# Performance work log

Measured on AMD Instinct MI355X. Metric: run time of the kernel, lower is better.

Reference implementation:

```python
import jax, jax.numpy as jnp
import numpy as np
from jax import lax

SUM_WEIGHT = 1.0
EPS = 1e-5
STRIDE = (2, 2, 2)
PAD = (1, 1, 1)
OUT_PAD = (1, 1, 1)
POOL = (2, 2, 2)


def setup_inputs() -> dict:
    key = jax.random.key(0)
    k1, k2, k3 = jax.random.split(key, 3)
    N, Cin, Cout = 32, 32, 64
    D, H, W = 16, 32, 32
    K = 3
    x = jax.random.normal(k1, (N, Cin, D, H, W), dtype=jnp.float32)
    fan_in = Cin * K * K * K
    w = jax.random.normal(k2, (Cin, Cout, K, K, K), dtype=jnp.float32) / np.sqrt(fan_in)
    b = jax.random.normal(k3, (Cout,), dtype=jnp.float32) * 0.01
    gamma = jnp.ones((Cout,), dtype=jnp.float32)
    beta = jnp.zeros((Cout,), dtype=jnp.float32)
    return {"x": x, "weight": w, "bias": b, "gamma": gamma, "beta": beta}


def _forward(x, weight, bias, gamma, beta):
    K = weight.shape[2]
    # ConvTranspose3d as correlation on stride-dilated input. The CUDA kernel
    # scatters with od = id*s - p + (K-1-kd) using weight[kd], i.e. the
    # spatially-flipped weight vs torch convT -> plain correlation here.
    pad_cfg = [(K - 1 - p, K - 1 - p + op) for p, op in zip(PAD, OUT_PAD)]
    y = lax.conv_general_dilated(
        x, weight,
        window_strides=(1, 1, 1),
        padding=pad_cfg,
        lhs_dilation=STRIDE,
        dimension_numbers=("NCDHW", "IODHW", "NCDHW"),
    )
    y = y + bias[None, :, None, None, None] + SUM_WEIGHT
    # Channel-wise LayerNorm: normalize over C at each (n, d, h, w), biased var.
    mean = jnp.mean(y, axis=1, keepdims=True)
    var = jnp.mean(jnp.square(y - mean), axis=1, keepdims=True)
    y = (y - mean) * lax.rsqrt(var + EPS)
    y = y * gamma[None, :, None, None, None] + beta[None, :, None, None, None]
    # AvgPool3d with kernel == stride == POOL via reshape + mean.
    N, C, Do, Ho, Wo = y.shape
    kd, kh, kw = POOL
    y = y.reshape(N, C, Do // kd, kd, Ho // kh, kh, Wo // kw, kw).mean(axis=(3, 5, 7))
    # GELU, tanh approximation (matches the CUDA kernel constants).
    c0 = jnp.float32(0.7978845608028654)
    c1 = jnp.float32(0.044715)
    return 0.5 * y * (1.0 + jnp.tanh(c0 * (y + c1 * y * y * y)))


def reference(x, weight, bias, gamma, beta):
    return _forward(x, weight, bias, gamma, beta)
```

## Files before the change

### kernel.cpp

```cpp
#include <hip/hip_runtime.h>
#include <math.h>


typedef __attribute__((ext_vector_type(8))) short short8;
typedef __attribute__((ext_vector_type(4))) float f32x4;

__device__ __forceinline__ unsigned short f2bf(float v) {
    unsigned int b = __float_as_uint(v);
    return (unsigned short)((b + 0x7fffu + ((b >> 16) & 1u)) >> 16);
}

__global__ void pack_w(const float* __restrict__ w, unsigned short* __restrict__ wp) {
    int t = blockIdx.x * 256 + threadIdx.x;
    if (t >= 27 * 64 * 32) return;
    int ci = t & 31, co = (t >> 5) & 63, tap = t >> 11;
    wp[(tap * 64 + co) * 32 + ci] = f2bf(w[(ci * 64 + co) * 27 + tap]);
}

__global__ __launch_bounds__(256, 2) void mfma_fused(
    const float* __restrict__ x, const unsigned short* __restrict__ wpack,
    const float* __restrict__ bias, const float* __restrict__ gamma,
    const float* __restrict__ beta, float* __restrict__ out)
{
    constexpr int COFF[9]   = {0, 1, 3, 5, 9, 11, 15, 19, 27};
    constexpr int TAPIDX[27] = {13, 12,14, 10,16, 9,11,15,17,
                                4,22, 3,5,21,23, 1,7,19,25,
                                0,2,6,8,18,20,24,26};
    constexpr int XROW[27]  = {0, 0,1, 0,33, 0,1,33,34,
                               0,99, 0,1,99,100, 0,33,99,132,
                               0,1,33,34,99,100,132,133};

    __shared__ unsigned short xs[6336];
    __shared__ float cbuf[2][64 * 68];

    const int t = threadIdx.x;
    const int lane = t & 63;
    const int wv = t >> 6;
    const int l15 = lane & 15;
    const int quad = lane >> 4;
    const int cobase = wv * 16;

    const int b = blockIdx.x;
    const int bq = b & 3;
    const int dp = (b >> 2) & 15;
    const int n = b >> 6;

    short8 Breg[27];
#pragma unroll
    for (int u = 0; u < 27; ++u)
        Breg[u] = *(const short8*)(wpack + (TAPIDX[u] * 64 + cobase + l15) * 32 + quad * 8);

    int base2[4], swzB[4];
#pragma unroll
    for (int s = 0; s < 4; ++s) {
        int m = s * 16 + l15;
        base2[s] = ((m >> 5) * 33 + (m & 31)) * 64;
    }
#pragma unroll
    for (int k = 0; k < 4; ++k)
        swzB[k] = (quad ^ ((l15 + k) & 3)) << 4;

    const float bco = bias[cobase + l15] + 1.0f;
    const int p = t >> 2, qq = t & 3;
    f32x4 gm[4], bt[4];
#pragma unroll
    for (int jj = 0; jj < 4; ++jj) {
        gm[jj] = *(const f32x4*)(gamma + qq * 16 + jj * 4);
        bt[jj] = *(const f32x4*)(beta + qq * 16 + jj * 4);
    }

    const char* xsb = (const char*)xs;

    for (int it = 0; it < 4; ++it) {
        const int hp0 = (bq * 4 + it) * 2;
        __syncthreads();

        for (int i = t; i < 792; i += 256) {
            int ww = i % 33;
            int g = i / 33;
            int chunk = g & 3;
            int gh = g >> 2;
            int dd = (gh >= 3) ? 1 : 0;
            int hh = gh - dd * 3;
            int row = gh * 33 + ww;
            int id = dp + dd, ih = hp0 + hh;
            short8 v8 = (short8)0;
            if (ww < 32 && ih < 32 && id < 16) {
                const float* xp = x + (((size_t)(n * 32 + chunk * 8) * 16 + id) << 10)
                                    + ih * 32 + ww;
#pragma unroll
                for (int j = 0; j < 8; ++j)
                    v8[j] = (short)f2bf(xp[(size_t)j << 14]);
            }
            *(short8*)((char*)xs + row * 64 + ((chunk ^ (row & 3)) << 4)) = v8;
        }
        __syncthreads();

        float pool[16];
#pragma unroll
        for (int j = 0; j < 16; ++j) pool[j] = 0.f;

#pragma unroll
        for (int c = 0; c < 8; ++c) {
            float* cb = cbuf[c & 1];
            f32x4 acc[4];
#pragma unroll
            for (int s = 0; s < 4; ++s) acc[s] = (f32x4)0.f;

#pragma unroll
            for (int u = COFF[c]; u < COFF[c + 1]; ++u) {
#pragma unroll
                for (int s = 0; s < 4; ++s) {
                    short8 a = *(const short8*)(xsb + base2[s]
                                + swzB[(XROW[u] + (s >> 1)) & 3] + XROW[u] * 64);
                    acc[s] = __builtin_amdgcn_mfma_f32_16x16x32_bf16(a, Breg[u], acc[s], 0, 0, 0);
                }
            }
#pragma unroll
            for (int s = 0; s < 4; ++s)
#pragma unroll
                for (int r = 0; r < 4; ++r)
                    cb[(s * 16 + quad * 4 + r) * 68 + cobase + l15] = acc[s][r] + bco;
            __syncthreads();

            f32x4 vv[4];
#pragma unroll
            for (int jj = 0; jj < 4; ++jj)
                vv[jj] = *(const f32x4*)&cb[p * 68 + qq * 16 + jj * 4];
            float s1 = 0.f, s2 = 0.f;
#pragma unroll
            for (int jj = 0; jj < 4; ++jj)
#pragma unroll
                for (int k = 0; k < 4; ++k) { float v = vv[jj][k]; s1 += v; s2 += v * v; }
            s1 += __shfl_xor(s1, 1); s2 += __shfl_xor(s2, 1);
            s1 += __shfl_xor(s1, 2); s2 += __shfl_xor(s2, 2);
            float mean = s1 * (1.f / 64.f);
            float var = s2 * (1.f / 64.f) - mean * mean;
            float rstd = rsqrtf(var + 1e-5f);
#pragma unroll
            for (int jj = 0; jj < 4; ++jj)
#pragma unroll
                for (int k = 0; k < 4; ++k)
                    pool[jj * 4 + k] += (vv[jj][k] - mean) * rstd;
        }

        float* eb = cbuf[0];
#pragma unroll
        for (int jj = 0; jj < 4; ++jj)
#pragma unroll
            for (int k = 0; k < 4; ++k) {
                float y = pool[jj * 4 + k] * 0.125f * gm[jj][k] + bt[jj][k];
                float u = 0.7978845608028654f * (y + 0.044715f * y * y * y);
                float g = y / (1.f + __expf(-2.f * u));
                eb[(qq * 16 + jj * 4 + k) * 65 + p] = g;
            }
        __syncthreads();
#pragma unroll
        for (int k2 = 0; k2 < 4; ++k2) {
            int idx = k2 * 256 + t;
            int c = idx >> 4;
            int pp = (idx & 15) * 4;
            f32x4 vq = *(const f32x4*)&eb[c * 65 + pp];
            *(f32x4*)&out[(((size_t)(n * 64 + c) * 16 + dp) << 10) + hp0 * 32 + pp] = vq;
        }
    }
}

__global__ __launch_bounds__(256) void fused_fallback(
    const float* __restrict__ x, const float* __restrict__ w,
    const float* __restrict__ bias, const float* __restrict__ gamma,
    const float* __restrict__ beta, float* __restrict__ out)
{
    __shared__ __align__(16) float xs_lds[128 * 20];
    __shared__ float conv_lds[128 * 65];
    float* stats = xs_lds;

    const int t = threadIdx.x;
    const int b = blockIdx.x;
    const int wq = b & 1;
    const int hp = (b >> 1) & 31;
    const int dp = (b >> 6) & 15;
    const int n = b >> 10;

    for (int k = 0; k < 10; ++k) {
        int idx = t + k * 256;
        int col = idx % 20, r = idx / 20;
        int hh = r & 1, ddv = (r >> 1) & 1, ci = r >> 2;
        int iw = wq * 16 + col, ih = hp + hh, id = dp + ddv;
        float v = 0.f;
        if (col < 17 && iw < 32 && ih < 32 && id < 16)
            v = x[(((n * 32 + ci) * 16 + id) * 32 + ih) * 32 + iw];
        xs_lds[idx] = v;
    }
    __syncthreads();

    const int co = t & 63;
    const int sg = t >> 6;
    const float bco = bias[co] + 1.0f;

    for (int dd = 0; dd < 2; ++dd)
        for (int hh = 0; hh < 2; ++hh) {
            float acc[8];
#pragma unroll
            for (int j = 0; j < 8; ++j) acc[j] = 0.f;
            const int ndt = dd ? 2 : 1, nht = hh ? 2 : 1;
            for (int itp = 0; itp < ndt; ++itp) {
                const int kd = dd ? (itp ? 2 : 0) : 1;
                const int idl = dd ? itp : 0;
                for (int jt = 0; jt < nht; ++jt) {
                    const int kh = hh ? (jt ? 2 : 0) : 1;
                    const int ihl = hh ? jt : 0;
                    const int kidx = kd * 3 + kh;
#pragma unroll 4
                    for (int ci = 0; ci < 32; ++ci) {
                        const float* wp0 = w + (ci * 64 + co) * 27 + kidx * 3;
                        float w0 = wp0[0], w1 = wp0[1], w2 = wp0[2];
                        const float* xr = &xs_lds[(ci * 4 + idl * 2 + ihl) * 20 + sg * 4];
                        float4 xa = *(const float4*)xr;
                        float x4 = xr[4];
                        acc[0] += xa.x * w1;
                        acc[1] += xa.x * w0 + xa.y * w2;
                        acc[2] += xa.y * w1;
                        acc[3] += xa.y * w0 + xa.z * w2;
                        acc[4] += xa.z * w1;
                        acc[5] += xa.z * w0 + xa.w * w2;
                        acc[6] += xa.w * w1;
                        acc[7] += xa.w * w0 + x4 * w2;
                    }
                }
            }
            const int posb = (dd * 2 + hh) * 32 + sg * 8;
#pragma unroll
            for (int j = 0; j < 8; ++j)
                conv_lds[(posb + j) * 65 + co] = acc[j] + bco;
        }
    __syncthreads();

    if (t < 128) {
        float s = 0.f, ss = 0.f;
#pragma unroll 8
        for (int c = 0; c < 64; ++c) { float v = conv_lds[t * 65 + c]; s += v; ss += v * v; }
        float mean = s * (1.f / 64.f);
        float var = ss * (1.f / 64.f) - mean * mean;
        stats[t] = mean;
        stats[128 + t] = rsqrtf(var + 1e-5f);
    }
    __syncthreads();

    {
        const int wp = t & 15, cog = t >> 4;
#pragma unroll
        for (int j = 0; j < 4; ++j) {
            const int c = cog * 4 + j;
            float sum = 0.f;
#pragma unroll
            for (int pd2 = 0; pd2 < 4; ++pd2)
#pragma unroll
                for (int ww = 0; ww < 2; ++ww) {
                    const int pos = pd2 * 32 + wp * 2 + ww;
                    sum += (conv_lds[pos * 65 + c] - stats[pos]) * stats[128 + pos];
                }
            float y = sum * 0.125f * gamma[c] + beta[c];
            float u = 0.7978845608028654f * (y + 0.044715f * y * y * y);
            float g = 0.5f * y * (1.f + tanhf(u));
            out[(((n * 64 + c) * 16 + dp) * 32 + hp) * 32 + (wq * 16 + wp)] = g;
        }
    }
}

extern "C" void kernel_launch(void* const* d_in, const int* in_sizes, int n_in,
                              void* d_out, int out_size, void* d_ws, size_t ws_size,
                              hipStream_t stream) {
    const float* x = (const float*)d_in[0];
    const float* w = (const float*)d_in[1];
    const float* bias = (const float*)d_in[2];
    const float* gamma = (const float*)d_in[3];
    const float* beta = (const float*)d_in[4];
    float* out = (float*)d_out;

    const size_t need = (size_t)(27 * 64 * 32) * sizeof(unsigned short);
    if (ws_size >= need) {
        unsigned short* wpack = (unsigned short*)d_ws;
        pack_w<<<(27 * 64 * 32 + 255) / 256, 256, 0, stream>>>(w, wpack);
        mfma_fused<<<2048, 256, 0, stream>>>(x, wpack, bias, gamma, beta, out);
    } else {
        fused_fallback<<<32768, 256, 0, stream>>>(x, w, bias, gamma, beta, out);
    }
}
```

Measured before the change: 329.3 us.

## Reorder transposed-conv MFMA loop to reuse each A fragment across parity classes

The MFMA loop is restructured. Each loaded input fragment (A operand) is reused for every output parity class that needs it, instead of being reloaded per class. Four parity accumulators are computed at once per spatial subtile, written to a larger LDS buffer, and then normalized per half. This cuts LDS reads of A fragments and halves the barrier count per class. The cost is more LDS (4x64x66 floats), which may lower occupancy, and more live accumulator registers.

```diff
diff --git a/kernel.cpp b/kernel.cpp
--- a/kernel.cpp
+++ b/kernel.cpp
@@ -22,16 +22,21 @@
     const float* __restrict__ bias, const float* __restrict__ gamma,
     const float* __restrict__ beta, float* __restrict__ out)
 {
-    constexpr int COFF[9]   = {0, 1, 3, 5, 9, 11, 15, 19, 27};
     constexpr int TAPIDX[27] = {13, 12,14, 10,16, 9,11,15,17,
                                 4,22, 3,5,21,23, 1,7,19,25,
                                 0,2,6,8,18,20,24,26};
-    constexpr int XROW[27]  = {0, 0,1, 0,33, 0,1,33,34,
-                               0,99, 0,1,99,100, 0,33,99,132,
-                               0,1,33,34,99,100,132,133};
+    constexpr int H_FR[12] = {0,1,33,34, 0,1,33,34,99,100,132,133};
+    constexpr int H_FO[13] = {0,4,6,8,9, 13,15,17,18,22,24,26,27};
+    constexpr int FL[3]    = {0,4,12};
+    constexpr int SEQ_U[27] = {0,1,3,5, 2,6, 4,7, 8,
+                               9,11,15,19, 12,20, 16,21, 22,
+                               10,13,17,23, 14,24, 18,25, 26};
+    constexpr int SEQ_C[27] = {0,1,2,3, 1,3, 2,3, 3,
+                               0,1,2,3, 1,3, 2,3, 3,
+                               0,1,2,3, 1,3, 2,3, 3};
 
     __shared__ unsigned short xs[6336];
-    __shared__ float cbuf[2][64 * 68];
+    __shared__ float cbuf[4 * 64 * 66];
 
     const int t = threadIdx.x;
     const int lane = t & 63;
@@ -101,50 +106,58 @@
         for (int j = 0; j < 16; ++j) pool[j] = 0.f;
 
 #pragma unroll
-        for (int c = 0; c < 8; ++c) {
-            float* cb = cbuf[c & 1];
-            f32x4 acc[4];
-#pragma unroll
-            for (int s = 0; s < 4; ++s) acc[s] = (f32x4)0.f;
-
-#pragma unroll
-            for (int u = COFF[c]; u < COFF[c + 1]; ++u) {
-#pragma unroll
-                for (int s = 0; s < 4; ++s) {
+        for (int half = 0; half < 2; ++half) {
+#pragma unroll
+            for (int s = 0; s < 4; ++s) {
+                f32x4 acc[4];
+#pragma unroll
+                for (int cc = 0; cc < 4; ++cc) acc[cc] = (f32x4)0.f;
+
+#pragma unroll
+                for (int f = FL[half]; f < FL[half + 1]; ++f) {
+                    const int F = H_FR[f];
                     short8 a = *(const short8*)(xsb + base2[s]
-                                + swzB[(XROW[u] + (s >> 1)) & 3] + XROW[u] * 64);
-                    acc[s] = __builtin_amdgcn_mfma_f32_16x16x32_bf16(a, Breg[u], acc[s], 0, 0, 0);
+                                + swzB[(F + (s >> 1)) & 3] + F * 64);
+#pragma unroll
+                    for (int i = H_FO[f]; i < H_FO[f + 1]; ++i)
+                        acc[SEQ_C[i]] = __builtin_amdgcn_mfma_f32_16x16x32_bf16(
+                            a, Breg[SEQ_U[i]], acc[SEQ_C[i]], 0, 0, 0);
                 }
-            }
-#pragma unroll
-            for (int s = 0; s < 4; ++s)
-#pragma unroll
-                for (int r = 0; r < 4; ++r)
-                    cb[(s * 16 + quad * 4 + r) * 68 + cobase + l15] = acc[s][r] + bco;
+#pragma unroll
+                for (int cc = 0; cc < 4; ++cc)
+#pragma unroll
+                    for (int r = 0; r < 4; ++r)
+                        cbuf[(cc * 64 + s * 16 + quad * 4 + r) * 66 + cobase + l15]
+                            = acc[cc][r] + bco;
+            }
             __syncthreads();
 
-            f32x4 vv[4];
-#pragma unroll
-            for (int jj = 0; jj < 4; ++jj)
-                vv[jj] = *(const f32x4*)&cb[p * 68 + qq * 16 + jj * 4];
-            float s1 = 0.f, s2 = 0.f;
-#pragma unroll
-            for (int jj = 0; jj < 4; ++jj)
-#pragma unroll
-                for (int k = 0; k < 4; ++k) { float v = vv[jj][k]; s1 += v; s2 += v * v; }
-            s1 += __shfl_xor(s1, 1); s2 += __shfl_xor(s2, 1);
-            s1 += __shfl_xor(s1, 2); s2 += __shfl_xor(s2, 2);
-            float mean = s1 * (1.f / 64.f);
-            float var = s2 * (1.f / 64.f) - mean * mean;
-            float rstd = rsqrtf(var + 1e-5f);
-#pragma unroll
-            for (int jj = 0; jj < 4; ++jj)
-#pragma unroll
-                for (int k = 0; k < 4; ++k)
-                    pool[jj * 4 + k] += (vv[jj][k] - mean) * rstd;
-        }
-
-        float* eb = cbuf[0];
+#pragma unroll
+            for (int cc = 0; cc < 4; ++cc) {
+                f32x4 vv[4];
+#pragma unroll
+                for (int jj = 0; jj < 4; ++jj)
+                    vv[jj] = *(const f32x4*)&cbuf[(cc * 64 + p) * 66 + qq * 16 + jj * 4];
+                float s1 = 0.f, s2 = 0.f;
+#pragma unroll
+                for (int jj = 0; jj < 4; ++jj)
+#pragma unroll
+                    for (int k = 0; k < 4; ++k) { float v = vv[jj][k]; s1 += v; s2 += v * v; }
+                s1 += __shfl_xor(s1, 1); s2 += __shfl_xor(s2, 1);
+                s1 += __shfl_xor(s1, 2); s2 += __shfl_xor(s2, 2);
+                float mean = s1 * (1.f / 64.f);
+                float var = s2 * (1.f / 64.f) - mean * mean;
+                float rstd = rsqrtf(var + 1e-5f);
+#pragma unroll
+                for (int jj = 0; jj < 4; ++jj)
+#pragma unroll
+                    for (int k = 0; k < 4; ++k)
+                        pool[jj * 4 + k] += (vv[jj][k] - mean) * rstd;
+            }
+            __syncthreads();
+        }
+
+        float* eb = cbuf;
 #pragma unroll
         for (int jj = 0; jj < 4; ++jj)
 #pragma unroll
```

After: 361.9 us. +9.9%, slower.
